# Kernel optimization log

Measured on AMD Instinct MI355X. Metric: run time of the kernel, lower is better.

The kernel has to match this reference:

```python
import jax, jax.numpy as jnp
import numpy as np

N_NODES = 50000


def setup_inputs() -> dict:
    key = jax.random.key(0)
    k1, k2, k3, k4 = jax.random.split(key, 4)
    x = jax.random.normal(k1, (N_NODES, 256), dtype=jnp.float32)
    edge_index = jax.random.randint(k2, (2, 800000), 0, N_NODES, dtype=jnp.int64)
    W1 = jax.random.normal(k3, (256, 128), dtype=jnp.float32) * (1.0 / np.sqrt(256))
    b1 = jnp.zeros((128,), dtype=jnp.float32)
    W2 = jax.random.normal(k4, (128, 16), dtype=jnp.float32) * (1.0 / np.sqrt(128))
    b2 = jnp.zeros((16,), dtype=jnp.float32)
    return {"x": x, "edge_index": edge_index, "W1": W1, "b1": b1, "W2": W2, "b2": b2}


def _gcn_norm(edge_index, num_nodes):
    # add self-loops, then symmetric normalization D^-1/2 A D^-1/2 (PyG GCNConv default)
    loop = jnp.arange(num_nodes, dtype=edge_index.dtype)
    src = jnp.concatenate([edge_index[0], loop])
    dst = jnp.concatenate([edge_index[1], loop])
    deg = jax.ops.segment_sum(jnp.ones_like(dst, dtype=jnp.float32), dst, num_segments=num_nodes)
    dinv = jnp.where(deg > 0, jax.lax.rsqrt(deg), 0.0)
    norm = dinv[src] * dinv[dst]  # [E+N]
    return src, dst, norm


def _gcn_conv(h, W, b, src, dst, norm, num_nodes):
    h = h @ W                             # linear before propagate
    msg = h[src] * norm[:, None]          # gather + edge scaling
    agg = jax.ops.segment_sum(msg, dst, num_segments=num_nodes)  # scatter-add
    return agg + b


def reference(x, edge_index, W1, b1, W2, b2):
    n = x.shape[0]
    src, dst, norm = _gcn_norm(edge_index, n)
    h = jax.nn.relu(_gcn_conv(x, W1, b1, src, dst, norm, n))
    # F.dropout(training=False) is identity in eval mode
    out = _gcn_conv(h, W2, b2, src, dst, norm, n)
    return jax.nn.log_softmax(out, axis=1)
```

## Files before the change

kernel.cpp:

```cpp
#include <hip/hip_runtime.h>
#include <hip/hip_bf16.h>
#include <math.h>


#define FIN 256
#define FH  128
#define FO  16
#define NCHUNK64 64
#define WPR_MAX 12544

typedef unsigned int uint;
typedef unsigned short ushort;
typedef __attribute__((ext_vector_type(8))) short bf16x8;
typedef __attribute__((ext_vector_type(4))) float f32x4;

static __device__ __forceinline__ ushort f2bf(float f) {
    __hip_bfloat16 b = __float2bfloat16(f);
    return *reinterpret_cast<ushort*>(&b);
}
static __device__ __forceinline__ float bf2f(ushort u) {
    return __uint_as_float(((uint)u) << 16);
}

__global__ __launch_bounds__(256) void GCN_wprep_k(const float* __restrict__ W1,
                                                   ushort* __restrict__ whT,
                                                   ushort* __restrict__ wlT) {
    int i = blockIdx.x * 256 + threadIdx.x;
    int k = i >> 7, c = i & 127;
    float w = W1[i];
    ushort hh = f2bf(w);
    ushort hl = f2bf(w - bf2f(hh));
    whT[c * 256 + k] = hh;
    wlT[c * 256 + k] = hl;
}

__global__ __launch_bounds__(256) void GCN_hist_k(const int* __restrict__ edge,
                                                  uint* __restrict__ cw,
                                                  int* __restrict__ rank,
                                                  int E, int ech,
                                                  int nWords, int wpr) {
    __shared__ uint lh[WPR_MAX];
    int tid = threadIdx.x;
    int r = blockIdx.x & 1;
    int c = blockIdx.x >> 1;
    int w0 = r * wpr;
    int wlim = nWords - w0; if (wlim > wpr) wlim = wpr;
    for (int j = tid; j < wlim; j += 256) lh[j] = 0;
    __syncthreads();
    int base = c * ech;
    int lim = base + ech; if (lim > E) lim = E;
    for (int i = base + tid; i < lim; i += 256) {
        int d = edge[E + i];
        int wd = (d >> 1) - w0;
        if ((unsigned)wd < (unsigned)wlim) {
            int sh = (d & 1) << 4;
            uint old = atomicAdd(&lh[wd], 1u << sh);
            rank[i] = (int)((old >> sh) & 0xFFFFu);
        }
    }
    __syncthreads();
    for (int j = tid; j < wlim; j += 256)
        cw[(size_t)c * nWords + w0 + j] = lh[j];
}

#define G1_BR 64
#define G1_KC 32

__global__ __launch_bounds__(256, 4) void GCN_gemm1_k(const float* __restrict__ x,
                                                      const ushort* __restrict__ whT,
                                                      const ushort* __restrict__ wlT,
                                                      ushort* __restrict__ h1,
                                                      int N) {
    __shared__ __align__(16) ushort xh_s[G1_BR * G1_KC];
    __shared__ __align__(16) ushort xl_s[G1_BR * G1_KC];
    __shared__ __align__(16) ushort wh_s[FH * G1_KC];
    __shared__ __align__(16) ushort wl_s[FH * G1_KC];
    int tid = threadIdx.x;

    int row0 = blockIdx.x * G1_BR;
    int ln = tid & 63;
    int w  = tid >> 6;
    int ln15 = ln & 15;
    int q16  = ln >> 4;

    f32x4 acc[4][2];
    #pragma unroll
    for (int mr = 0; mr < 4; mr++)
        #pragma unroll
        for (int nc = 0; nc < 2; nc++) acc[mr][nc] = (f32x4){0.f, 0.f, 0.f, 0.f};

    for (int kc = 0; kc < FIN; kc += G1_KC) {
        #pragma unroll
        for (int j = 0; j < 2; j++) {
            int u = tid + j * 256;
            int r = u >> 3, kq = u & 7;
            int gr = row0 + r;
            float4 v = make_float4(0.f, 0.f, 0.f, 0.f);
            if (gr < N) v = *(const float4*)&x[(size_t)gr * FIN + kc + kq * 4];
            ushort h0 = f2bf(v.x), h1v = f2bf(v.y), h2 = f2bf(v.z), h3 = f2bf(v.w);
            ushort l0 = f2bf(v.x - bf2f(h0));
            ushort l1 = f2bf(v.y - bf2f(h1v));
            ushort l2 = f2bf(v.z - bf2f(h2));
            ushort l3 = f2bf(v.w - bf2f(h3));
            uint2 hw, lw;
            hw.x = (uint)h0 | ((uint)h1v << 16);
            hw.y = (uint)h2 | ((uint)h3 << 16);
            lw.x = (uint)l0 | ((uint)l1 << 16);
            lw.y = (uint)l2 | ((uint)l3 << 16);
            int byte = (r * 64 + kq * 8) ^ (((r >> 1) & 3) << 4);
            *(uint2*)((char*)xh_s + byte) = hw;
            *(uint2*)((char*)xl_s + byte) = lw;
        }
        #pragma unroll
        for (int j = 0; j < 2; j++) {
            int u = tid + j * 256;
            int c = u >> 2, ku = u & 3;
            uint4 vh = *(const uint4*)&whT[(size_t)c * 256 + kc + ku * 8];
            uint4 vl = *(const uint4*)&wlT[(size_t)c * 256 + kc + ku * 8];
            int byte = (c * 64 + ku * 16) ^ (((c >> 1) & 3) << 4);
            *(uint4*)((char*)wh_s + byte) = vh;
            *(uint4*)((char*)wl_s + byte) = vl;
        }
        __syncthreads();

        bf16x8 ah[4], al[4], bh[2], bl[2];
        #pragma unroll
        for (int mr = 0; mr < 4; mr++) {
            int r = mr * 16 + ln15;
            int byte = r * 64 + ((q16 * 16) ^ (((r >> 1) & 3) << 4));
            ah[mr] = *(const bf16x8*)((const char*)xh_s + byte);
            al[mr] = *(const bf16x8*)((const char*)xl_s + byte);
        }
        #pragma unroll
        for (int nc = 0; nc < 2; nc++) {
            int c = w * 32 + nc * 16 + ln15;
            int byte = c * 64 + ((q16 * 16) ^ (((c >> 1) & 3) << 4));
            bh[nc] = *(const bf16x8*)((const char*)wh_s + byte);
            bl[nc] = *(const bf16x8*)((const char*)wl_s + byte);
        }
        #pragma unroll
        for (int mr = 0; mr < 4; mr++)
            #pragma unroll
            for (int nc = 0; nc < 2; nc++) {
                acc[mr][nc] = __builtin_amdgcn_mfma_f32_16x16x32_bf16(
                    ah[mr], bh[nc], acc[mr][nc], 0, 0, 0);
                acc[mr][nc] = __builtin_amdgcn_mfma_f32_16x16x32_bf16(
                    al[mr], bh[nc], acc[mr][nc], 0, 0, 0);
                acc[mr][nc] = __builtin_amdgcn_mfma_f32_16x16x32_bf16(
                    ah[mr], bl[nc], acc[mr][nc], 0, 0, 0);
            }
        __syncthreads();
    }

    #pragma unroll
    for (int mr = 0; mr < 4; mr++) {
        #pragma unroll
        for (int nc = 0; nc < 2; nc++) {
            int cw2 = w * 32 + nc * 16 + ln15;
            #pragma unroll
            for (int j = 0; j < 4; j++) {
                int gr = row0 + mr * 16 + q16 * 4 + j;
                if (gr < N) h1[(size_t)gr * FH + cw2] = f2bf(acc[mr][nc][j]);
            }
        }
    }
}

__global__ __launch_bounds__(256) void GCN_chpfx_k(uint* __restrict__ cw,
                                                   int* __restrict__ count,
                                                   int* __restrict__ bsum,
                                                   int N, int nWords) {
    int tid = threadIdx.x;
    int w = blockIdx.x * 256 + tid;
    int local = 0;
    if (w < nWords) {
        uint re = 0, ro = 0;
        #pragma unroll 8
        for (int c = 0; c < NCHUNK64; c++) {
            uint* p = &cw[(size_t)c * nWords + w];
            uint v = *p;
            *p = re | (ro << 16);
            re += v & 0xFFFFu;
            ro += v >> 16;
        }
        int d0 = 2 * w;
        if (d0 < N)     { count[d0]     = (int)re; local += (int)re + 1; }
        if (d0 + 1 < N) { count[d0 + 1] = (int)ro; local += (int)ro + 1; }
    }
    __shared__ int red[256];
    red[tid] = local;
    __syncthreads();
    for (int st = 64; st > 0; st >>= 1) {
        if ((tid & 127) < st) red[tid] += red[tid + st];
        __syncthreads();
    }
    if (tid == 0)   bsum[blockIdx.x * 2 + 0] = red[0];
    if (tid == 128) bsum[blockIdx.x * 2 + 1] = red[128];
}

__global__ __launch_bounds__(256) void GCN_scan2_k(const int* __restrict__ count,
                                                   const int* __restrict__ bsum,
                                                   int2* __restrict__ rd2,
                                                   int2* __restrict__ edata, int N) {
    int tid = threadIdx.x;
    int b = blockIdx.x;
    int d = b * 256 + tid;
    int cnt1 = (d < N) ? count[d] + 1 : 0;

    __shared__ int red[256];
    int offp = 0;
    for (int t = tid; t < b; t += 256) offp += bsum[t];
    red[tid] = offp;
    __syncthreads();
    for (int st = 128; st > 0; st >>= 1) {
        if (tid < st) red[tid] += red[tid + st];
        __syncthreads();
    }
    int blockOff = red[0];
    __syncthreads();

    __shared__ int ssum[256];
    ssum[tid] = cnt1;
    __syncthreads();
    for (int off = 1; off < 256; off <<= 1) {
        int t = (tid >= off) ? ssum[tid - off] : 0;
        __syncthreads();
        ssum[tid] += t;
        __syncthreads();
    }
    int r = blockOff + ssum[tid] - cnt1;

    if (d < N) {
        float dv = rsqrtf((float)cnt1);
        rd2[d] = make_int2(r, __float_as_int(dv));
        edata[r] = make_int2(d, __float_as_int(dv * dv));
    }
    if (b == gridDim.x - 1 && tid == 255) rd2[N] = make_int2(blockOff + ssum[255], 0);
}

__global__ __launch_bounds__(256) void GCN_fill_k(const int* __restrict__ edge,
                                                  const int* __restrict__ rank,
                                                  const uint* __restrict__ cw,
                                                  const int2* __restrict__ rd2,
                                                  int2* __restrict__ edata,
                                                  int E, int ech, int nWords) {
    int i = blockIdx.x * 256 + threadIdx.x;
    if (i >= E) return;
    int s = edge[i];
    int d = edge[E + i];
    int rk = rank[i];
    int c = i / ech;
    uint pw = cw[(size_t)c * nWords + (d >> 1)];
    int pfx = (int)((pw >> ((d & 1) << 4)) & 0xFFFFu);
    int2 rdd = rd2[d];
    float ds = __int_as_float(rd2[s].y);
    edata[rdd.x + 1 + pfx + rk] =
        make_int2(s, __float_as_int(ds * __int_as_float(rdd.y)));
}

__global__ __launch_bounds__(256) void GCN_agg1gemm2_k(
        const ushort* __restrict__ h1, const int2* __restrict__ rd2,
        const int2* __restrict__ ed, const float* __restrict__ b1,
        const float* __restrict__ W2, ushort* __restrict__ h2b, int N) {
    __shared__ float w2s[FH][FO];
    __shared__ float hs[16][FH + 4];
    int tid = threadIdx.x;
    #pragma unroll
    for (int j = 0; j < (FH * FO) / 256; j++) {
        int i = tid + j * 256;
        w2s[i >> 4][i & 15] = W2[i];
    }

    int node0 = blockIdx.x * 16;
    int local = tid >> 4;
    int j = tid & 15;
    int node = node0 + local;

    if (node < N) {
        int beg = rd2[node].x, end = rd2[node + 1].x;
        const uint4* hp = (const uint4*)h1;

        float a[8];
        #pragma unroll
        for (int t = 0; t < 8; t++) a[t] = 0.f;

        int i = beg;
        for (; i + 4 <= end; i += 4) {
            int2 e0 = ed[i + 0], e1 = ed[i + 1], e2 = ed[i + 2], e3 = ed[i + 3];
            float w0 = __int_as_float(e0.y), w1 = __int_as_float(e1.y);
            float w2 = __int_as_float(e2.y), w3 = __int_as_float(e3.y);
            uint4 g0 = hp[(size_t)e0.x * 16 + j];
            uint4 g1 = hp[(size_t)e1.x * 16 + j];
            uint4 g2 = hp[(size_t)e2.x * 16 + j];
            uint4 g3 = hp[(size_t)e3.x * 16 + j];
            #pragma unroll
            for (int q = 0; q < 4; q++) {
                uint u0 = (&g0.x)[q], u1 = (&g1.x)[q], u2 = (&g2.x)[q], u3 = (&g3.x)[q];
                a[q*2+0] += __uint_as_float(u0 << 16) * w0;
                a[q*2+1] += __uint_as_float(u0 & 0xFFFF0000u) * w0;
                a[q*2+0] += __uint_as_float(u1 << 16) * w1;
                a[q*2+1] += __uint_as_float(u1 & 0xFFFF0000u) * w1;
                a[q*2+0] += __uint_as_float(u2 << 16) * w2;
                a[q*2+1] += __uint_as_float(u2 & 0xFFFF0000u) * w2;
                a[q*2+0] += __uint_as_float(u3 << 16) * w3;
                a[q*2+1] += __uint_as_float(u3 & 0xFFFF0000u) * w3;
            }
        }
        for (; i < end; i++) {
            int2 e = ed[i];
            float w = __int_as_float(e.y);
            uint4 g = hp[(size_t)e.x * 16 + j];
            #pragma unroll
            for (int q = 0; q < 4; q++) {
                uint u = (&g.x)[q];
                a[q*2+0] += __uint_as_float(u << 16) * w;
                a[q*2+1] += __uint_as_float(u & 0xFFFF0000u) * w;
            }
        }

        const float4* bp = (const float4*)b1;
        float4 bb0 = bp[j * 2 + 0];
        float4 bb1 = bp[j * 2 + 1];
        float4 o0, o1;
        o0.x = fmaxf(a[0] + bb0.x, 0.f);
        o0.y = fmaxf(a[1] + bb0.y, 0.f);
        o0.z = fmaxf(a[2] + bb0.z, 0.f);
        o0.w = fmaxf(a[3] + bb0.w, 0.f);
        o1.x = fmaxf(a[4] + bb1.x, 0.f);
        o1.y = fmaxf(a[5] + bb1.y, 0.f);
        o1.z = fmaxf(a[6] + bb1.z, 0.f);
        o1.w = fmaxf(a[7] + bb1.w, 0.f);
        *(float4*)&hs[local][j * 8 + 0] = o0;
        *(float4*)&hs[local][j * 8 + 4] = o1;
    }
    __syncthreads();

    float acc = 0.f;
    #pragma unroll 8
    for (int k = 0; k < FH; k++) acc += hs[local][k] * w2s[k][j];
    if (node < N) h2b[(size_t)node * FO + j] = f2bf(acc);
}

__global__ __launch_bounds__(256) void GCN_agg2_k(const ushort* __restrict__ h2b,
                                                  const int2* __restrict__ rd2,
                                                  const int2* __restrict__ ed,
                                                  const float* __restrict__ b2,
                                                  float* __restrict__ out, int N) {
    int tid = threadIdx.x;
    int node = blockIdx.x * 32 + (tid >> 3);
    if (node >= N) return;
    int f2 = tid & 7;
    int beg = rd2[node].x, end = rd2[node + 1].x;
    const uint* hp = (const uint*)h2b;
    float a0 = 0.f, a1 = 0.f;
    int i = beg;
    for (; i + 4 <= end; i += 4) {
        int2 e0 = ed[i + 0], e1 = ed[i + 1], e2 = ed[i + 2], e3 = ed[i + 3];
        uint u0 = hp[(size_t)e0.x * 8 + f2];
        uint u1 = hp[(size_t)e1.x * 8 + f2];
        uint u2 = hp[(size_t)e2.x * 8 + f2];
        uint u3 = hp[(size_t)e3.x * 8 + f2];
        float w0 = __int_as_float(e0.y), w1 = __int_as_float(e1.y);
        float w2 = __int_as_float(e2.y), w3 = __int_as_float(e3.y);
        a0 += __uint_as_float(u0 << 16) * w0 + __uint_as_float(u1 << 16) * w1
            + __uint_as_float(u2 << 16) * w2 + __uint_as_float(u3 << 16) * w3;
        a1 += __uint_as_float(u0 & 0xFFFF0000u) * w0 + __uint_as_float(u1 & 0xFFFF0000u) * w1
            + __uint_as_float(u2 & 0xFFFF0000u) * w2 + __uint_as_float(u3 & 0xFFFF0000u) * w3;
    }
    for (; i < end; i++) {
        int2 e = ed[i];
        uint u = hp[(size_t)e.x * 8 + f2];
        float w = __int_as_float(e.y);
        a0 += __uint_as_float(u << 16) * w;
        a1 += __uint_as_float(u & 0xFFFF0000u) * w;
    }
    float2 bb = ((const float2*)b2)[f2];
    float v0 = a0 + bb.x;
    float v1 = a1 + bb.y;
    float mx = fmaxf(v0, v1);
    #pragma unroll
    for (int m = 4; m >= 1; m >>= 1) mx = fmaxf(mx, __shfl_xor(mx, m, 8));
    float s = expf(v0 - mx) + expf(v1 - mx);
    #pragma unroll
    for (int m = 4; m >= 1; m >>= 1) s += __shfl_xor(s, m, 8);
    float ls = logf(s);
    float2 o = make_float2(v0 - mx - ls, v1 - mx - ls);
    ((float2*)out)[(size_t)node * 8 + f2] = o;
}

extern "C" void kernel_launch(void* const* d_in, const int* in_sizes, int n_in,
                              void* d_out, int out_size, void* d_ws, size_t ws_size,
                              hipStream_t stream) {
    (void)n_in; (void)out_size; (void)ws_size;
    const float* x  = (const float*)d_in[0];
    const int*   edp = (const int*)d_in[1];
    const float* W1 = (const float*)d_in[2];
    const float* b1 = (const float*)d_in[3];
    const float* W2 = (const float*)d_in[4];
    const float* b2 = (const float*)d_in[5];
    float* out = (float*)d_out;

    int N = in_sizes[0] / FIN;
    int E = in_sizes[1] / 2;
    int M = E + N;
    int nWords = (N + 1) / 2;
    int wpr = (nWords + 1) / 2;
    int ech = (E + NCHUNK64 - 1) / NCHUNK64;
    int nScanBlocks = (N + 255) / 256;
    int nChpfx = (nWords + 255) / 256;

    char* p = (char*)d_ws;
    auto take = [&](size_t bytes) -> char* {
        char* r = p;
        p += (bytes + 255) & ~(size_t)255;
        return r;
    };
    int*    count  = (int*)take((size_t)N * 4);
    int*    rank   = (int*)take((size_t)E * 4);
    uint*   cw     = (uint*)take((size_t)NCHUNK64 * nWords * 4);
    int2*   rd2    = (int2*)take((size_t)(N + 1) * 8);
    int*    bsum   = (int*)take((size_t)(2 * nChpfx) * 4);
    int2*   edata  = (int2*)take((size_t)M * 8);
    ushort* whT    = (ushort*)take((size_t)FH * FIN * 2);
    ushort* wlT    = (ushort*)take((size_t)FH * FIN * 2);
    ushort* h1     = (ushort*)take((size_t)N * FH * 2);
    ushort* h2b    = (ushort*)take((size_t)N * FO * 2);

    int eBlocks = (E + 255) / 256;
    int nGemm   = (N + G1_BR - 1) / G1_BR;

    GCN_wprep_k<<<(FIN * FH) / 256, 256, 0, stream>>>(W1, whT, wlT);
    GCN_hist_k<<<2 * NCHUNK64, 256, 0, stream>>>(edp, cw, rank, E, ech, nWords, wpr);
    GCN_gemm1_k<<<nGemm, 256, 0, stream>>>(x, whT, wlT, h1, N);
    GCN_chpfx_k<<<nChpfx, 256, 0, stream>>>(cw, count, bsum, N, nWords);
    GCN_scan2_k<<<nScanBlocks, 256, 0, stream>>>(count, bsum, rd2, edata, N);
    GCN_fill_k<<<eBlocks, 256, 0, stream>>>(edp, rank, cw, rd2, edata, E, ech, nWords);
    GCN_agg1gemm2_k<<<(N + 15) / 16, 256, 0, stream>>>(h1, rd2, edata, b1, W2, h2b, N);
    GCN_agg2_k<<<(N + 31) / 32, 256, 0, stream>>>(h2b, rd2, edata, b2, out, N);
}
```

Before: 130.6 us.

## Merge histogram and GEMM1 into one launch and double histogram chunks

The edge-degree histogram kernel and the first bf16-split GEMM are combined into a single launch. The first blocks build histograms and the rest compute GEMM tiles, so the two independent stages share the device instead of running back to back. The histogram chunk count grows from 64 to 128, which gives more histogram blocks to run alongside the GEMM but makes the prefix kernel scan twice as many chunk rows. Every block now reserves the full 50 KB shared buffer and the launch-bounds occupancy hint of 4 is dropped, so fewer GEMM blocks fit per CU.

```diff
diff --git a/kernel.cpp b/kernel.cpp
--- a/kernel.cpp
+++ b/kernel.cpp
@@ -6,7 +6,7 @@
 #define FIN 256
 #define FH  128
 #define FO  16
-#define NCHUNK64 64
+#define NCHUNK 128
 #define WPR_MAX 12544
 
 typedef unsigned int uint;
@@ -34,50 +34,49 @@
     wlT[c * 256 + k] = hl;
 }
 
-__global__ __launch_bounds__(256) void GCN_hist_k(const int* __restrict__ edge,
-                                                  uint* __restrict__ cw,
-                                                  int* __restrict__ rank,
-                                                  int E, int ech,
-                                                  int nWords, int wpr) {
-    __shared__ uint lh[WPR_MAX];
-    int tid = threadIdx.x;
-    int r = blockIdx.x & 1;
-    int c = blockIdx.x >> 1;
-    int w0 = r * wpr;
-    int wlim = nWords - w0; if (wlim > wpr) wlim = wpr;
-    for (int j = tid; j < wlim; j += 256) lh[j] = 0;
-    __syncthreads();
-    int base = c * ech;
-    int lim = base + ech; if (lim > E) lim = E;
-    for (int i = base + tid; i < lim; i += 256) {
-        int d = edge[E + i];
-        int wd = (d >> 1) - w0;
-        if ((unsigned)wd < (unsigned)wlim) {
-            int sh = (d & 1) << 4;
-            uint old = atomicAdd(&lh[wd], 1u << sh);
-            rank[i] = (int)((old >> sh) & 0xFFFFu);
-        }
-    }
-    __syncthreads();
-    for (int j = tid; j < wlim; j += 256)
-        cw[(size_t)c * nWords + w0 + j] = lh[j];
-}
-
 #define G1_BR 64
 #define G1_KC 32
 
-__global__ __launch_bounds__(256, 4) void GCN_gemm1_k(const float* __restrict__ x,
-                                                      const ushort* __restrict__ whT,
-                                                      const ushort* __restrict__ wlT,
-                                                      ushort* __restrict__ h1,
-                                                      int N) {
-    __shared__ __align__(16) ushort xh_s[G1_BR * G1_KC];
-    __shared__ __align__(16) ushort xl_s[G1_BR * G1_KC];
-    __shared__ __align__(16) ushort wh_s[FH * G1_KC];
-    __shared__ __align__(16) ushort wl_s[FH * G1_KC];
+__global__ __launch_bounds__(256) void GCN_histgemm_k(
+        const float* __restrict__ x, const ushort* __restrict__ whT,
+        const ushort* __restrict__ wlT, ushort* __restrict__ h1,
+        const int* __restrict__ edge, uint* __restrict__ cw,
+        int* __restrict__ rank,
+        int N, int E, int nHist, int ech, int nWords, int wpr) {
+    __shared__ __align__(16) char smem[WPR_MAX * 4];
     int tid = threadIdx.x;
 
-    int row0 = blockIdx.x * G1_BR;
+    if ((int)blockIdx.x < nHist) {
+        int bid = blockIdx.x;
+        int r = bid & 1;
+        int c = bid >> 1;
+        uint* lh = (uint*)smem;
+        int w0 = r * wpr;
+        int wlim = nWords - w0; if (wlim > wpr) wlim = wpr;
+        for (int j = tid; j < wlim; j += 256) lh[j] = 0;
+        __syncthreads();
+        int base = c * ech;
+        int lim = base + ech; if (lim > E) lim = E;
+        for (int i = base + tid; i < lim; i += 256) {
+            int d = edge[E + i];
+            int wd = (d >> 1) - w0;
+            if ((unsigned)wd < (unsigned)wlim) {
+                int sh = (d & 1) << 4;
+                uint old = atomicAdd(&lh[wd], 1u << sh);
+                rank[i] = (int)((old >> sh) & 0xFFFFu);
+            }
+        }
+        __syncthreads();
+        for (int j = tid; j < wlim; j += 256)
+            cw[(size_t)c * nWords + w0 + j] = lh[j];
+        return;
+    }
+
+    ushort* xh_s = (ushort*)smem;
+    ushort* xl_s = (ushort*)(smem + 4096);
+    ushort* wh_s = (ushort*)(smem + 8192);
+    ushort* wl_s = (ushort*)(smem + 16384);
+    int row0 = (blockIdx.x - nHist) * G1_BR;
     int ln = tid & 63;
     int w  = tid >> 6;
     int ln15 = ln & 15;
@@ -176,7 +175,7 @@
     if (w < nWords) {
         uint re = 0, ro = 0;
         #pragma unroll 8
-        for (int c = 0; c < NCHUNK64; c++) {
+        for (int c = 0; c < NCHUNK; c++) {
             uint* p = &cw[(size_t)c * nWords + w];
             uint v = *p;
             *p = re | (ro << 16);
@@ -405,7 +404,7 @@
     int M = E + N;
     int nWords = (N + 1) / 2;
     int wpr = (nWords + 1) / 2;
-    int ech = (E + NCHUNK64 - 1) / NCHUNK64;
+    int ech = (E + NCHUNK - 1) / NCHUNK;
     int nScanBlocks = (N + 255) / 256;
     int nChpfx = (nWords + 255) / 256;
 
@@ -417,7 +416,7 @@
     };
     int*    count  = (int*)take((size_t)N * 4);
     int*    rank   = (int*)take((size_t)E * 4);
-    uint*   cw     = (uint*)take((size_t)NCHUNK64 * nWords * 4);
+    uint*   cw     = (uint*)take((size_t)NCHUNK * nWords * 4);
     int2*   rd2    = (int2*)take((size_t)(N + 1) * 8);
     int*    bsum   = (int*)take((size_t)(2 * nChpfx) * 4);
     int2*   edata  = (int2*)take((size_t)M * 8);
@@ -428,10 +427,11 @@
 
     int eBlocks = (E + 255) / 256;
     int nGemm   = (N + G1_BR - 1) / G1_BR;
+    int nHist   = 2 * NCHUNK;
 
     GCN_wprep_k<<<(FIN * FH) / 256, 256, 0, stream>>>(W1, whT, wlT);
-    GCN_hist_k<<<2 * NCHUNK64, 256, 0, stream>>>(edp, cw, rank, E, ech, nWords, wpr);
-    GCN_gemm1_k<<<nGemm, 256, 0, stream>>>(x, whT, wlT, h1, N);
+    GCN_histgemm_k<<<nHist + nGemm, 256, 0, stream>>>(
+        x, whT, wlT, h1, edp, cw, rank, N, E, nHist, ech, nWords, wpr);
     GCN_chpfx_k<<<nChpfx, 256, 0, stream>>>(cw, count, bsum, N, nWords);
     GCN_scan2_k<<<nScanBlocks, 256, 0, stream>>>(count, bsum, rd2, edata, N);
     GCN_fill_k<<<eBlocks, 256, 0, stream>>>(edp, rank, cw, rd2, edata, E, ech, nWords);
```

Measured after the change: 131.2 us. No clear change (+0.4%).
